# Optimization experiments

Hardware: AMD Instinct MI355X
Metric: run time of the kernel (lower is better)

The kernel has to match this reference:

```python
import jax, jax.numpy as jnp
import numpy as np

N = 50000        # nodes
E = 800000       # edges
IN_FEAT = 128
OUT_FEAT = 64
HEADS = 4
NUM_CLASSES = 40
NEG_SLOPE = 0.2  # DGL GATConv default


def setup_inputs() -> dict:
    key = jax.random.key(0)
    ks = jax.random.split(key, 12)
    x = jax.random.normal(ks[0], (N, IN_FEAT), dtype=jnp.float32)
    src = jax.random.randint(ks[1], (E,), 0, N, dtype=jnp.int32)
    dst = jax.random.randint(ks[2], (E,), 0, N, dtype=jnp.int32)
    # layer 1 params: fc W1 [in, H*D], attn_l/attn_r [H, D], bias [H*D]
    s1 = 1.0 / np.sqrt(IN_FEAT)
    W1 = jax.random.normal(ks[3], (IN_FEAT, HEADS * OUT_FEAT), dtype=jnp.float32) * s1
    al1 = jax.random.normal(ks[4], (HEADS, OUT_FEAT), dtype=jnp.float32) * 0.1
    ar1 = jax.random.normal(ks[5], (HEADS, OUT_FEAT), dtype=jnp.float32) * 0.1
    b1 = jnp.zeros((HEADS * OUT_FEAT,), dtype=jnp.float32)
    # layer 2 params: fc W2 [H*D, C], attn [1, C], bias [C]
    hid = HEADS * OUT_FEAT
    s2 = 1.0 / np.sqrt(hid)
    W2 = jax.random.normal(ks[6], (hid, NUM_CLASSES), dtype=jnp.float32) * s2
    al2 = jax.random.normal(ks[7], (1, NUM_CLASSES), dtype=jnp.float32) * 0.1
    ar2 = jax.random.normal(ks[8], (1, NUM_CLASSES), dtype=jnp.float32) * 0.1
    b2 = jnp.zeros((NUM_CLASSES,), dtype=jnp.float32)
    return {"x": x, "src": src, "dst": dst,
            "W1": W1, "al1": al1, "ar1": ar1, "b1": b1,
            "W2": W2, "al2": al2, "ar2": ar2, "b2": b2}


def gat_layer(x, W, al, ar, bias, src, dst, heads, out_feat):
    n = x.shape[0]
    h = (x @ W).reshape(n, heads, out_feat)            # [N,H,D]
    el = jnp.sum(h * al[None], axis=-1)                # [N,H]
    er = jnp.sum(h * ar[None], axis=-1)                # [N,H]
    e = el[src] + er[dst]                              # [E,H]
    e = jnp.where(e > 0, e, NEG_SLOPE * e)             # LeakyReLU
    # segment softmax over edges sharing the same destination
    emax = jax.ops.segment_max(e, dst, num_segments=n)           # [N,H]
    emax = jnp.where(jnp.isfinite(emax), emax, 0.0)              # isolated nodes
    ee = jnp.exp(e - emax[dst])                                  # [E,H]
    denom = jax.ops.segment_sum(ee, dst, num_segments=n)         # [N,H]
    denom = jnp.where(denom > 0, denom, 1.0)
    alpha = ee / denom[dst]                                      # [E,H]
    msg = h[src] * alpha[:, :, None]                             # [E,H,D]
    out = jax.ops.segment_sum(msg, dst, num_segments=n)          # [N,H,D]
    return out + bias.reshape(1, heads, out_feat)


def reference(x, src, dst, W1, al1, ar1, b1, W2, al2, ar2, b2):
    h = gat_layer(x, W1, al1, ar1, b1, src, dst, HEADS, OUT_FEAT)  # [N,H,D]
    h = h.reshape(h.shape[0], HEADS * OUT_FEAT)
    h = jax.nn.elu(h)
    h = gat_layer(h, W2, al2, ar2, b2, src, dst, 1, NUM_CLASSES)   # [N,1,C]
    return jnp.squeeze(h, axis=1)                                   # [N,C]
```

## Files before the change

kernel.cpp:

```cpp
#include <hip/hip_runtime.h>

#define NN 50000
#define NE 800000
#define HID 256
#define NCLS 40

typedef short bf16x8 __attribute__((ext_vector_type(8)));
typedef float f32x4 __attribute__((ext_vector_type(4)));

__device__ inline unsigned short f2bf(float f) {
    unsigned int u = __float_as_uint(f);
    return (unsigned short)((u + 0x7FFFu + ((u >> 16) & 1u)) >> 16);
}
__device__ inline unsigned int pack2bf(float a, float b) {
    return (unsigned int)f2bf(a) | ((unsigned int)f2bf(b) << 16);
}
__device__ inline float2 bf2x(unsigned int u) {
    return make_float2(__uint_as_float(u << 16), __uint_as_float(u & 0xFFFF0000u));
}

__global__ void k_scanA(const int* __restrict__ counts, int* __restrict__ indptr,
                        int* __restrict__ bsum) {
    __shared__ int sh[256];
    int t = threadIdx.x;
    int idx = blockIdx.x * 256 + t;
    int c = idx < NN ? counts[idx] : 0;
    sh[t] = c;
    __syncthreads();
    for (int off = 1; off < 256; off <<= 1) {
        int v = (t >= off) ? sh[t - off] : 0;
        __syncthreads();
        sh[t] += v;
        __syncthreads();
    }
    if (idx < NN) indptr[idx] = sh[t] - c;
    if (t == 255) bsum[blockIdx.x] = sh[255];
}

__global__ void k_scanB(int* __restrict__ bsum, int nb) {
    __shared__ int sh[256];
    int t = threadIdx.x;
    int c = t < nb ? bsum[t] : 0;
    sh[t] = c;
    __syncthreads();
    for (int off = 1; off < 256; off <<= 1) {
        int v = (t >= off) ? sh[t - off] : 0;
        __syncthreads();
        sh[t] += v;
        __syncthreads();
    }
    if (t < nb) bsum[t] = sh[t] - c;
}

__global__ void k_scanC(int* __restrict__ indptr, const int* __restrict__ bsum,
                        int* __restrict__ fill) {
    int idx = blockIdx.x * 256 + threadIdx.x;
    if (idx < NN) {
        indptr[idx] += bsum[idx >> 8];
        fill[idx] = 0;
    }
    if (idx == 0) indptr[NN] = NE;
}

__global__ void k_scatterw(const int* __restrict__ src, const int* __restrict__ dst,
                           const int* __restrict__ indptr, int* __restrict__ fill,
                           const float* __restrict__ el1, const float* __restrict__ er1,
                           int* __restrict__ srcs, float4* __restrict__ w4) {
    int e = blockIdx.x * 256 + threadIdx.x;
    if (e < NE) {
        int d = dst[e];
        int s = src[e];
        int pos = atomicAdd(&fill[d], 1);
        int j = indptr[d] + pos;
        srcs[j] = s;
        float4 ls = *(const float4*)&el1[(size_t)s * 4];
        float4 rd = *(const float4*)&er1[(size_t)d * 4];
        float e0 = ls.x + rd.x, e1 = ls.y + rd.y, e2 = ls.z + rd.z, e3 = ls.w + rd.w;
        e0 = e0 > 0.f ? e0 : 0.2f * e0;
        e1 = e1 > 0.f ? e1 : 0.2f * e1;
        e2 = e2 > 0.f ? e2 : 0.2f * e2;
        e3 = e3 > 0.f ? e3 : 0.2f * e3;
        w4[j] = make_float4(__expf(e0), __expf(e1), __expf(e2), __expf(e3));
    }
}

__global__ void k_prep(const float* __restrict__ W1, const float* __restrict__ al,
                       const float* __restrict__ ar, const float* __restrict__ W2,
                       float* __restrict__ wel, float* __restrict__ wer,
                       unsigned short* __restrict__ W1Tb,
                       unsigned short* __restrict__ W2Tb,
                       int* __restrict__ counts) {
    int gid = blockIdx.x * 256 + threadIdx.x;
    int nth = gridDim.x * 256;
    const int TOT = 512 + 32768 + 48 * 256;
    for (int i = gid; i < TOT; i += nth) {
        if (i < 512) {
            int k = i >> 2, h = i & 3;
            float a = 0.f, b = 0.f;
            for (int dd = 0; dd < 64; ++dd) {
                float w = W1[k * 256 + h * 64 + dd];
                a = fmaf(w, al[h * 64 + dd], a);
                b = fmaf(w, ar[h * 64 + dd], b);
            }
            wel[i] = a;
            wer[i] = b;
        } else if (i < 512 + 32768) {
            int j = i - 512;
            int col = j >> 7, k = j & 127;
            W1Tb[j] = f2bf(W1[k * 256 + col]);
        } else {
            int j = i - 512 - 32768;
            int col = j >> 8, kk = j & 255;
            W2Tb[j] = (col < NCLS) ? f2bf(W2[kk * 40 + col]) : (unsigned short)0;
        }
    }
    for (int i = gid; i < NN; i += nth) counts[i] = 0;
}

__global__ void k_elr1x(const float* __restrict__ x, const float* __restrict__ wel,
                        const float* __restrict__ wer, float* __restrict__ el1,
                        float* __restrict__ er1, unsigned short* __restrict__ xb,
                        const int* __restrict__ dst, int* __restrict__ counts) {
    __shared__ float xs[64 * 129];
    __shared__ float wels[512], wers[512];
    int t = threadIdx.x;
    int n0 = blockIdx.x * 64;
    wels[t] = wel[t]; wels[256 + t] = wel[256 + t];
    wers[t] = wer[t]; wers[256 + t] = wer[256 + t];
    for (int i = 0; i < 8; ++i) {
        int f = i * 256 + t;
        int row = f >> 5;
        int col4 = (f & 31) * 4;
        float4 v = make_float4(0.f, 0.f, 0.f, 0.f);
        if (n0 + row < NN) v = ((const float4*)x)[(size_t)n0 * 32 + f];
        xs[row * 129 + col4 + 0] = v.x;
        xs[row * 129 + col4 + 1] = v.y;
        xs[row * 129 + col4 + 2] = v.z;
        xs[row * 129 + col4 + 3] = v.w;
    }
    __syncthreads();
    int node = t & 63;
    int h = t >> 6;
    float a = 0.f, b = 0.f;
    for (int k = 0; k < 128; ++k) {
        float xv = xs[node * 129 + k];
        a = fmaf(xv, wels[k * 4 + h], a);
        b = fmaf(xv, wers[k * 4 + h], b);
    }
    if (n0 + node < NN) {
        el1[(size_t)(n0 + node) * 4 + h] = a;
        er1[(size_t)(n0 + node) * 4 + h] = b;
    }
    for (int i = 0; i < 4; ++i) {
        int g = (i * 256 + t) * 8;
        int row = g >> 7, col = g & 127;
        if (n0 + row < NN) {
            ushort4 lo, hi;
            lo.x = f2bf(xs[row * 129 + col + 0]);
            lo.y = f2bf(xs[row * 129 + col + 1]);
            lo.z = f2bf(xs[row * 129 + col + 2]);
            lo.w = f2bf(xs[row * 129 + col + 3]);
            hi.x = f2bf(xs[row * 129 + col + 4]);
            hi.y = f2bf(xs[row * 129 + col + 5]);
            hi.z = f2bf(xs[row * 129 + col + 6]);
            hi.w = f2bf(xs[row * 129 + col + 7]);
            *(ushort4*)&xb[(size_t)(n0 + row) * 128 + col] = lo;
            *(ushort4*)&xb[(size_t)(n0 + row) * 128 + col + 4] = hi;
        }
    }
    int gid = blockIdx.x * 256 + t;
    int nth = gridDim.x * 256;
    for (int e = gid; e < NE; e += nth) atomicAdd(&counts[dst[e]], 1);
}

#define XG_STRIDE 260
#define EB_STRIDE 264
#define FMA8(AC0, AC1, AC2, AC3, WQ, XV) \
    AC0.x = fmaf(WQ.x, XV.x, AC0.x); AC0.y = fmaf(WQ.x, XV.y, AC0.y); \
    AC1.x = fmaf(WQ.y, XV.x, AC1.x); AC1.y = fmaf(WQ.y, XV.y, AC1.y); \
    AC2.x = fmaf(WQ.z, XV.x, AC2.x); AC2.y = fmaf(WQ.z, XV.y, AC2.y); \
    AC3.x = fmaf(WQ.w, XV.x, AC3.x); AC3.y = fmaf(WQ.w, XV.y, AC3.y);

__global__ void k_agg1m(const unsigned int* __restrict__ xb32,
                        const float4* __restrict__ w4,
                        const int* __restrict__ indptr, const int* __restrict__ srcs,
                        const unsigned short* __restrict__ W1Tb,
                        const unsigned short* __restrict__ W2Tb,
                        const float* __restrict__ b1,
                        const float* __restrict__ al2, const float* __restrict__ ar2,
                        unsigned short* __restrict__ h2b,
                        float* __restrict__ el2, float* __restrict__ er2) {
    __shared__ unsigned int xg[16 * XG_STRIDE];
    __shared__ __align__(16) unsigned char pool[10496];
    float4 (*sw)[64] = (float4(*)[64])pool;
    int (*si)[64] = (int(*)[64])(pool + 8192);
    unsigned short* eb = (unsigned short*)pool;
    float* pel = (float*)(pool + 8448);
    float* per_ = (float*)(pool + 8640);
    int t = threadIdx.x;
    int wv = t >> 6, l = t & 63;
    int n0 = blockIdx.x * 16;
    int d0 = n0 + wv * 4;
    int ip[5];
#pragma unroll
    for (int q = 0; q < 5; ++q) ip[q] = indptr[d0 + q];
    int w2 = wv * 2;
#pragma unroll
    for (int p = 0; p < 2; ++p) {
        int begA = ip[2 * p + 0], endA = ip[2 * p + 1];
        int begB = ip[2 * p + 1], endB = ip[2 * p + 2];
        int degA = endA - begA, degB = endB - begB;
        int sA = 0, sB = 0;
        float4 wA = make_float4(0.f, 0.f, 0.f, 0.f);
        float4 wB = make_float4(0.f, 0.f, 0.f, 0.f);
        if (l < degA) { sA = srcs[begA + l]; wA = w4[begA + l]; }
        if (l < degB) { sB = srcs[begB + l]; wB = w4[begB + l]; }
        si[w2 + 0][l] = sA; sw[w2 + 0][l] = wA;
        si[w2 + 1][l] = sB; sw[w2 + 1][l] = wB;
        float2 aA0 = {0,0}, aA1 = {0,0}, aA2 = {0,0}, aA3 = {0,0};
        float2 aB0 = {0,0}, aB1 = {0,0}, aB2 = {0,0}, aB3 = {0,0};
        int capA = degA < 64 ? degA : 64;
        int capB = degB < 64 ? degB : 64;
        int mcap = capA > capB ? capA : capB;
        for (int e = 0; e < mcap; e += 8) {
            unsigned int uA[8], uB[8];
            bool doA = e < capA, doB = e < capB;
            if (doA) {
#pragma unroll
                for (int q = 0; q < 8; ++q)
                    uA[q] = xb32[(size_t)si[w2][e + q] * 64 + l];
            }
            if (doB) {
#pragma unroll
                for (int q = 0; q < 8; ++q)
                    uB[q] = xb32[(size_t)si[w2 + 1][e + q] * 64 + l];
            }
            if (doA) {
#pragma unroll
                for (int q = 0; q < 8; ++q) {
                    float4 wq = sw[w2][e + q];
                    float2 xv = bf2x(uA[q]);
                    FMA8(aA0, aA1, aA2, aA3, wq, xv)
                }
            }
            if (doB) {
#pragma unroll
                for (int q = 0; q < 8; ++q) {
                    float4 wq = sw[w2 + 1][e + q];
                    float2 xv = bf2x(uB[q]);
                    FMA8(aB0, aB1, aB2, aB3, wq, xv)
                }
            }
        }
        for (int j = begA + 64; j < endA; ++j) {
            float4 wq = w4[j];
            float2 xv = bf2x(xb32[(size_t)srcs[j] * 64 + l]);
            FMA8(aA0, aA1, aA2, aA3, wq, xv)
        }
        for (int j = begB + 64; j < endB; ++j) {
            float4 wq = w4[j];
            float2 xv = bf2x(xb32[(size_t)srcs[j] * 64 + l]);
            FMA8(aB0, aB1, aB2, aB3, wq, xv)
        }
        float dA0 = wA.x, dA1 = wA.y, dA2 = wA.z, dA3 = wA.w;
        float dB0 = wB.x, dB1 = wB.y, dB2 = wB.z, dB3 = wB.w;
        for (int j = begA + 64 + l; j < endA; j += 64) {
            float4 wt = w4[j];
            dA0 += wt.x; dA1 += wt.y; dA2 += wt.z; dA3 += wt.w;
        }
        for (int j = begB + 64 + l; j < endB; j += 64) {
            float4 wt = w4[j];
            dB0 += wt.x; dB1 += wt.y; dB2 += wt.z; dB3 += wt.w;
        }
#pragma unroll
        for (int off = 32; off > 0; off >>= 1) {
            dA0 += __shfl_xor(dA0, off); dA1 += __shfl_xor(dA1, off);
            dA2 += __shfl_xor(dA2, off); dA3 += __shfl_xor(dA3, off);
            dB0 += __shfl_xor(dB0, off); dB1 += __shfl_xor(dB1, off);
            dB2 += __shfl_xor(dB2, off); dB3 += __shfl_xor(dB3, off);
        }
        float iA0 = dA0 > 0.f ? 1.f / dA0 : 0.f;
        float iA1 = dA1 > 0.f ? 1.f / dA1 : 0.f;
        float iA2 = dA2 > 0.f ? 1.f / dA2 : 0.f;
        float iA3 = dA3 > 0.f ? 1.f / dA3 : 0.f;
        float iB0 = dB0 > 0.f ? 1.f / dB0 : 0.f;
        float iB1 = dB1 > 0.f ? 1.f / dB1 : 0.f;
        float iB2 = dB2 > 0.f ? 1.f / dB2 : 0.f;
        float iB3 = dB3 > 0.f ? 1.f / dB3 : 0.f;
        unsigned int* xgA = &xg[(wv * 4 + 2 * p + 0) * XG_STRIDE];
        xgA[0 * 64 + l] = pack2bf(aA0.x * iA0, aA0.y * iA0);
        xgA[1 * 64 + l] = pack2bf(aA1.x * iA1, aA1.y * iA1);
        xgA[2 * 64 + l] = pack2bf(aA2.x * iA2, aA2.y * iA2);
        xgA[3 * 64 + l] = pack2bf(aA3.x * iA3, aA3.y * iA3);
        unsigned int* xgB = &xg[(wv * 4 + 2 * p + 1) * XG_STRIDE];
        xgB[0 * 64 + l] = pack2bf(aB0.x * iB0, aB0.y * iB0);
        xgB[1 * 64 + l] = pack2bf(aB1.x * iB1, aB1.y * iB1);
        xgB[2 * 64 + l] = pack2bf(aB2.x * iB2, aB2.y * iB2);
        xgB[3 * 64 + l] = pack2bf(aB3.x * iB3, aB3.y * iB3);
    }
    __syncthreads();
    int lrow = l & 15, lk = l >> 4;
    {
        f32x4 acc[4] = {};
#pragma unroll
        for (int kt = 0; kt < 4; ++kt) {
            bf16x8 av = *(const bf16x8*)&xg[lrow * XG_STRIDE + wv * 64 + kt * 16 + lk * 4];
#pragma unroll
            for (int nt = 0; nt < 4; ++nt) {
                int col = wv * 64 + nt * 16 + lrow;
                bf16x8 bv = *(const bf16x8*)&W1Tb[(size_t)col * 128 + kt * 32 + lk * 8];
                acc[nt] = __builtin_amdgcn_mfma_f32_16x16x32_bf16(av, bv, acc[nt], 0, 0, 0);
            }
        }
#pragma unroll
        for (int nt = 0; nt < 4; ++nt) {
            int col = wv * 64 + nt * 16 + lrow;
            float bv1 = b1[col];
#pragma unroll
            for (int r = 0; r < 4; ++r) {
                int rloc = lk * 4 + r;
                float o = acc[nt][r] + bv1;
                o = o > 0.f ? o : (__expf(o) - 1.f);
                eb[rloc * EB_STRIDE + col] = f2bf(o);
            }
        }
    }
    __syncthreads();
    if (wv < 3) {
        f32x4 acc2 = {};
#pragma unroll
        for (int kt = 0; kt < 8; ++kt) {
            bf16x8 av = *(const bf16x8*)&eb[lrow * EB_STRIDE + kt * 32 + lk * 8];
            bf16x8 bv = *(const bf16x8*)&W2Tb[(size_t)(wv * 16 + lrow) * 256 + kt * 32 + lk * 8];
            acc2 = __builtin_amdgcn_mfma_f32_16x16x32_bf16(av, bv, acc2, 0, 0, 0);
        }
        int col2 = wv * 16 + lrow;
        float alc = col2 < NCLS ? al2[col2] : 0.f;
        float arc = col2 < NCLS ? ar2[col2] : 0.f;
#pragma unroll
        for (int r = 0; r < 4; ++r) {
            int row = n0 + lk * 4 + r;
            float v = acc2[r];
            if (col2 < NCLS) h2b[(size_t)row * NCLS + col2] = f2bf(v);
            float pa = v * alc, pb = v * arc;
#pragma unroll
            for (int off = 1; off < 16; off <<= 1) {
                pa += __shfl_xor(pa, off);
                pb += __shfl_xor(pb, off);
            }
            if (lrow == 0) {
                pel[wv * 16 + lk * 4 + r] = pa;
                per_[wv * 16 + lk * 4 + r] = pb;
            }
        }
    }
    __syncthreads();
    if (t < 16) {
        el2[n0 + t] = pel[t] + pel[16 + t] + pel[32 + t];
        er2[n0 + t] = per_[t] + per_[16 + t] + per_[32 + t];
    }
}

__global__ void k_agg2(const unsigned int* __restrict__ h2b32,
                       const float* __restrict__ el2,
                       const float* __restrict__ er2, const float* __restrict__ b2,
                       const int* __restrict__ indptr, const int* __restrict__ srcs,
                       float* __restrict__ out) {
    __shared__ int   si[8][64];
    __shared__ float sw[8][64];
    int t = threadIdx.x;
    int wv = t >> 6, l = t & 63;
    int dA = blockIdx.x * 8 + wv * 2;
    int dB = dA + 1;
    int begA = indptr[dA], endA = indptr[dA + 1];
    int begB = endA, endB = indptr[dB + 1];
    int degA = endA - begA, degB = endB - begB;
    float rdA = er2[dA], rdB = er2[dB];
    int sA = 0, sB = 0;
    float wA = 0.f, wB = 0.f;
    if (l < degA) {
        sA = srcs[begA + l];
        float e = el2[sA] + rdA;
        e = e > 0.f ? e : 0.2f * e;
        wA = __expf(e);
    }
    if (l < degB) {
        sB = srcs[begB + l];
        float e = el2[sB] + rdB;
        e = e > 0.f ? e : 0.2f * e;
        wB = __expf(e);
    }
    int w2 = wv * 2;
    si[w2 + 0][l] = sA; sw[w2 + 0][l] = wA;
    si[w2 + 1][l] = sB; sw[w2 + 1][l] = wB;
    float denA = wA, denB = wB;
    for (int j = begA + 64 + l; j < endA; j += 64) {
        float e = el2[srcs[j]] + rdA;
        e = e > 0.f ? e : 0.2f * e;
        denA += __expf(e);
    }
    for (int j = begB + 64 + l; j < endB; j += 64) {
        float e = el2[srcs[j]] + rdB;
        e = e > 0.f ? e : 0.2f * e;
        denB += __expf(e);
    }
    int half = l >> 5, il = l & 31;
    bool act = il < 20;
    float2 accA = {0.f, 0.f}, accB = {0.f, 0.f};
    int capA = degA < 64 ? degA : 64;
    int capB = degB < 64 ? degB : 64;
    int mcap = capA > capB ? capA : capB;
    for (int e = 0; e < mcap; e += 8) {
        bool doA = e < capA, doB = e < capB;
        int ixA[4], ixB[4];
        float wsA[4], wsB[4];
        unsigned int uA[4], uB[4];
        if (doA) {
#pragma unroll
            for (int q = 0; q < 4; ++q) {
                int idx = e + 2 * q + half;
                ixA[q] = si[w2][idx];
                wsA[q] = sw[w2][idx];
            }
        }
        if (doB) {
#pragma unroll
            for (int q = 0; q < 4; ++q) {
                int idx = e + 2 * q + half;
                ixB[q] = si[w2 + 1][idx];
                wsB[q] = sw[w2 + 1][idx];
            }
        }
        if (doA) {
#pragma unroll
            for (int q = 0; q < 4; ++q)
                uA[q] = act ? h2b32[(size_t)ixA[q] * 20 + il] : 0u;
        }
        if (doB) {
#pragma unroll
            for (int q = 0; q < 4; ++q)
                uB[q] = act ? h2b32[(size_t)ixB[q] * 20 + il] : 0u;
        }
        if (doA) {
#pragma unroll
            for (int q = 0; q < 4; ++q) {
                float2 xv = bf2x(uA[q]);
                accA.x = fmaf(wsA[q], xv.x, accA.x);
                accA.y = fmaf(wsA[q], xv.y, accA.y);
            }
        }
        if (doB) {
#pragma unroll
            for (int q = 0; q < 4; ++q) {
                float2 xv = bf2x(uB[q]);
                accB.x = fmaf(wsB[q], xv.x, accB.x);
                accB.y = fmaf(wsB[q], xv.y, accB.y);
            }
        }
    }
    for (int j = begA + 64; j < endA; ++j) {
        int s = srcs[j];
        float e = el2[s] + rdA;
        e = e > 0.f ? e : 0.2f * e;
        float ww = (half == 0) ? __expf(e) : 0.f;
        unsigned int u = act ? h2b32[(size_t)s * 20 + il] : 0u;
        float2 xv = bf2x(u);
        accA.x = fmaf(ww, xv.x, accA.x);
        accA.y = fmaf(ww, xv.y, accA.y);
    }
    for (int j = begB + 64; j < endB; ++j) {
        int s = srcs[j];
        float e = el2[s] + rdB;
        e = e > 0.f ? e : 0.2f * e;
        float ww = (half == 0) ? __expf(e) : 0.f;
        unsigned int u = act ? h2b32[(size_t)s * 20 + il] : 0u;
        float2 xv = bf2x(u);
        accB.x = fmaf(ww, xv.x, accB.x);
        accB.y = fmaf(ww, xv.y, accB.y);
    }
#pragma unroll
    for (int off = 32; off > 0; off >>= 1) {
        denA += __shfl_xor(denA, off);
        denB += __shfl_xor(denB, off);
    }
    float invA = denA > 0.f ? 1.f / denA : 0.f;
    float invB = denB > 0.f ? 1.f / denB : 0.f;
    accA.x += __shfl_xor(accA.x, 32);
    accA.y += __shfl_xor(accA.y, 32);
    accB.x += __shfl_xor(accB.x, 32);
    accB.y += __shfl_xor(accB.y, 32);
    if (half == 0 && act) {
        float2 bb = *(const float2*)&b2[2 * il];
        *(float2*)&out[(size_t)dA * NCLS + 2 * il] =
            make_float2(fmaf(accA.x, invA, bb.x), fmaf(accA.y, invA, bb.y));
        *(float2*)&out[(size_t)dB * NCLS + 2 * il] =
            make_float2(fmaf(accB.x, invB, bb.x), fmaf(accB.y, invB, bb.y));
    }
}

extern "C" void kernel_launch(void* const* d_in, const int* in_sizes, int n_in,
                              void* d_out, int out_size, void* d_ws, size_t ws_size,
                              hipStream_t stream) {
    const float* x   = (const float*)d_in[0];
    const int*   src = (const int*)d_in[1];
    const int*   dst = (const int*)d_in[2];
    const float* W1  = (const float*)d_in[3];
    const float* al1 = (const float*)d_in[4];
    const float* ar1 = (const float*)d_in[5];
    const float* b1  = (const float*)d_in[6];
    const float* W2  = (const float*)d_in[7];
    const float* al2 = (const float*)d_in[8];
    const float* ar2 = (const float*)d_in[9];
    const float* b2  = (const float*)d_in[10];
    float* out = (float*)d_out;

    float* ws = (float*)d_ws;
    size_t off = 0;
    unsigned short* xb    = (unsigned short*)(ws + off); off += (size_t)NN * 64;
    unsigned short* h2b   = (unsigned short*)(ws + off); off += (size_t)NN * 20;
    float* el1  = ws + off; off += (size_t)NN * 4;
    float* er1  = ws + off; off += (size_t)NN * 4;
    float* el2  = ws + off; off += NN;
    float* er2  = ws + off; off += NN;
    float* wel  = ws + off; off += 512;
    float* wer  = ws + off; off += 512;
    unsigned short* w1tb = (unsigned short*)(ws + off); off += 16384;
    unsigned short* w2tb = (unsigned short*)(ws + off); off += 48 * 128;
    float* w4   = ws + off; off += (size_t)NE * 4;
    int* counts = (int*)(ws + off);
    int* indptr = counts + NN;
    int* fill   = indptr + NN + 1;
    int* srcs   = fill + NN;
    int* bsum   = srcs + NE;

    const int NB = (NN + 255) / 256;

    k_prep<<<48, 256, 0, stream>>>(W1, al1, ar1, W2, wel, wer, w1tb, w2tb, counts);
    k_elr1x<<<(NN + 63) / 64, 256, 0, stream>>>(x, wel, wer, el1, er1, xb, dst, counts);
    k_scanA<<<NB, 256, 0, stream>>>(counts, indptr, bsum);
    k_scanB<<<1, 256, 0, stream>>>(bsum, NB);
    k_scanC<<<NB, 256, 0, stream>>>(indptr, bsum, fill);
    k_scatterw<<<(NE + 255) / 256, 256, 0, stream>>>(src, dst, indptr, fill,
                                                     el1, er1, srcs, (float4*)w4);
    k_agg1m<<<NN / 16, 256, 0, stream>>>((const unsigned int*)xb, (const float4*)w4,
                                         indptr, srcs, w1tb, w2tb, b1, al2, ar2,
                                         h2b, el2, er2);

    k_agg2<<<NN / 8, 256, 0, stream>>>((const unsigned int*)h2b, el2, er2, b2,
                                       indptr, srcs, out);
}
```

Before: 197.6 us.

## Sort destination nodes by in-degree to balance aggregation workloads

Builds a degree histogram during the scan, prefix-sums it, and counting-sorts the node ids into a permutation grouped by in-degree. Both aggregation kernels then assign each wave or block a group of nodes with similar degree, which cuts the divergence and idle lanes that come from mixing short and long neighbour lists. In exchange it adds global atomics for the histogram and placement, and indirection reads. Node outputs are now scattered writes rather than contiguous ones, and locality across neighbouring nodes' indptr entries is lost.

```diff
diff --git a/kernel.cpp b/kernel.cpp
--- a/kernel.cpp
+++ b/kernel.cpp
@@ -20,7 +20,7 @@
 }
 
 __global__ void k_scanA(const int* __restrict__ counts, int* __restrict__ indptr,
-                        int* __restrict__ bsum) {
+                        int* __restrict__ bsum, int* __restrict__ dhist) {
     __shared__ int sh[256];
     int t = threadIdx.x;
     int idx = blockIdx.x * 256 + t;
@@ -33,11 +33,15 @@
         sh[t] += v;
         __syncthreads();
     }
-    if (idx < NN) indptr[idx] = sh[t] - c;
+    if (idx < NN) {
+        indptr[idx] = sh[t] - c;
+        int b = c < 255 ? c : 255;
+        atomicAdd(&dhist[b], 1);
+    }
     if (t == 255) bsum[blockIdx.x] = sh[255];
 }
 
-__global__ void k_scanB(int* __restrict__ bsum, int nb) {
+__global__ void k_scanB(int* __restrict__ bsum, int nb, int* __restrict__ dhist) {
     __shared__ int sh[256];
     int t = threadIdx.x;
     int c = t < nb ? bsum[t] : 0;
@@ -50,14 +54,31 @@
         __syncthreads();
     }
     if (t < nb) bsum[t] = sh[t] - c;
+    __syncthreads();
+    int h = dhist[t];
+    sh[t] = h;
+    __syncthreads();
+    for (int off = 1; off < 256; off <<= 1) {
+        int v = (t >= off) ? sh[t - off] : 0;
+        __syncthreads();
+        sh[t] += v;
+        __syncthreads();
+    }
+    dhist[t] = sh[t] - h;
 }
 
 __global__ void k_scanC(int* __restrict__ indptr, const int* __restrict__ bsum,
-                        int* __restrict__ fill) {
+                        int* __restrict__ fill, const int* __restrict__ counts,
+                        const int* __restrict__ dhist, int* __restrict__ dfill,
+                        int* __restrict__ perm) {
     int idx = blockIdx.x * 256 + threadIdx.x;
     if (idx < NN) {
         indptr[idx] += bsum[idx >> 8];
         fill[idx] = 0;
+        int c = counts[idx];
+        int b = c < 255 ? c : 255;
+        int pos = atomicAdd(&dfill[b], 1);
+        perm[dhist[b] + pos] = idx;
     }
     if (idx == 0) indptr[NN] = NE;
 }
@@ -89,7 +110,8 @@
                        float* __restrict__ wel, float* __restrict__ wer,
                        unsigned short* __restrict__ W1Tb,
                        unsigned short* __restrict__ W2Tb,
-                       int* __restrict__ counts) {
+                       int* __restrict__ counts, int* __restrict__ dhist,
+                       int* __restrict__ dfill) {
     int gid = blockIdx.x * 256 + threadIdx.x;
     int nth = gridDim.x * 256;
     const int TOT = 512 + 32768 + 48 * 256;
@@ -115,6 +137,7 @@
         }
     }
     for (int i = gid; i < NN; i += nth) counts[i] = 0;
+    if (gid < 256) { dhist[gid] = 0; dfill[gid] = 0; }
 }
 
 __global__ void k_elr1x(const float* __restrict__ x, const float* __restrict__ wel,
@@ -184,6 +207,7 @@
 __global__ void k_agg1m(const unsigned int* __restrict__ xb32,
                         const float4* __restrict__ w4,
                         const int* __restrict__ indptr, const int* __restrict__ srcs,
+                        const int* __restrict__ perm,
                         const unsigned short* __restrict__ W1Tb,
                         const unsigned short* __restrict__ W2Tb,
                         const float* __restrict__ b1,
@@ -192,6 +216,7 @@
                         float* __restrict__ el2, float* __restrict__ er2) {
     __shared__ unsigned int xg[16 * XG_STRIDE];
     __shared__ __align__(16) unsigned char pool[10496];
+    __shared__ int pp[16];
     float4 (*sw)[64] = (float4(*)[64])pool;
     int (*si)[64] = (int(*)[64])(pool + 8192);
     unsigned short* eb = (unsigned short*)pool;
@@ -201,14 +226,20 @@
     int wv = t >> 6, l = t & 63;
     int n0 = blockIdx.x * 16;
     int d0 = n0 + wv * 4;
-    int ip[5];
-#pragma unroll
-    for (int q = 0; q < 5; ++q) ip[q] = indptr[d0 + q];
+    if (t < 16) pp[t] = perm[n0 + t];
+    int pm4[4], ipb[4], ipe[4];
+#pragma unroll
+    for (int q = 0; q < 4; ++q) pm4[q] = perm[d0 + q];
+#pragma unroll
+    for (int q = 0; q < 4; ++q) {
+        ipb[q] = indptr[pm4[q]];
+        ipe[q] = indptr[pm4[q] + 1];
+    }
     int w2 = wv * 2;
 #pragma unroll
     for (int p = 0; p < 2; ++p) {
-        int begA = ip[2 * p + 0], endA = ip[2 * p + 1];
-        int begB = ip[2 * p + 1], endB = ip[2 * p + 2];
+        int begA = ipb[2 * p + 0], endA = ipe[2 * p + 0];
+        int begB = ipb[2 * p + 1], endB = ipe[2 * p + 1];
         int degA = endA - begA, degB = endB - begB;
         int sA = 0, sB = 0;
         float4 wA = make_float4(0.f, 0.f, 0.f, 0.f);
@@ -339,7 +370,8 @@
         float arc = col2 < NCLS ? ar2[col2] : 0.f;
 #pragma unroll
         for (int r = 0; r < 4; ++r) {
-            int row = n0 + lk * 4 + r;
+            int rloc = lk * 4 + r;
+            int row = pp[rloc];
             float v = acc2[r];
             if (col2 < NCLS) h2b[(size_t)row * NCLS + col2] = f2bf(v);
             float pa = v * alc, pb = v * arc;
@@ -349,15 +381,16 @@
                 pb += __shfl_xor(pb, off);
             }
             if (lrow == 0) {
-                pel[wv * 16 + lk * 4 + r] = pa;
-                per_[wv * 16 + lk * 4 + r] = pb;
+                pel[wv * 16 + rloc] = pa;
+                per_[wv * 16 + rloc] = pb;
             }
         }
     }
     __syncthreads();
     if (t < 16) {
-        el2[n0 + t] = pel[t] + pel[16 + t] + pel[32 + t];
-        er2[n0 + t] = per_[t] + per_[16 + t] + per_[32 + t];
+        int row = pp[t];
+        el2[row] = pel[t] + pel[16 + t] + pel[32 + t];
+        er2[row] = per_[t] + per_[16 + t] + per_[32 + t];
     }
 }
 
@@ -365,15 +398,17 @@
                        const float* __restrict__ el2,
                        const float* __restrict__ er2, const float* __restrict__ b2,
                        const int* __restrict__ indptr, const int* __restrict__ srcs,
+                       const int* __restrict__ perm,
                        float* __restrict__ out) {
     __shared__ int   si[8][64];
     __shared__ float sw[8][64];
     int t = threadIdx.x;
     int wv = t >> 6, l = t & 63;
-    int dA = blockIdx.x * 8 + wv * 2;
-    int dB = dA + 1;
+    int base8 = blockIdx.x * 8;
+    int dA = perm[base8 + wv * 2];
+    int dB = perm[base8 + wv * 2 + 1];
     int begA = indptr[dA], endA = indptr[dA + 1];
-    int begB = endA, endB = indptr[dB + 1];
+    int begB = indptr[dB], endB = indptr[dB + 1];
     int degA = endA - begA, degB = endB - begB;
     float rdA = er2[dA], rdB = er2[dB];
     int sA = 0, sB = 0;
@@ -532,20 +567,24 @@
     int* fill   = indptr + NN + 1;
     int* srcs   = fill + NN;
     int* bsum   = srcs + NE;
+    int* dhist  = bsum + 256;
+    int* dfill  = dhist + 256;
+    int* perm   = dfill + 256;
 
     const int NB = (NN + 255) / 256;
 
-    k_prep<<<48, 256, 0, stream>>>(W1, al1, ar1, W2, wel, wer, w1tb, w2tb, counts);
+    k_prep<<<48, 256, 0, stream>>>(W1, al1, ar1, W2, wel, wer, w1tb, w2tb,
+                                   counts, dhist, dfill);
     k_elr1x<<<(NN + 63) / 64, 256, 0, stream>>>(x, wel, wer, el1, er1, xb, dst, counts);
-    k_scanA<<<NB, 256, 0, stream>>>(counts, indptr, bsum);
-    k_scanB<<<1, 256, 0, stream>>>(bsum, NB);
-    k_scanC<<<NB, 256, 0, stream>>>(indptr, bsum, fill);
+    k_scanA<<<NB, 256, 0, stream>>>(counts, indptr, bsum, dhist);
+    k_scanB<<<1, 256, 0, stream>>>(bsum, NB, dhist);
+    k_scanC<<<NB, 256, 0, stream>>>(indptr, bsum, fill, counts, dhist, dfill, perm);
     k_scatterw<<<(NE + 255) / 256, 256, 0, stream>>>(src, dst, indptr, fill,
                                                      el1, er1, srcs, (float4*)w4);
     k_agg1m<<<NN / 16, 256, 0, stream>>>((const unsigned int*)xb, (const float4*)w4,
-                                         indptr, srcs, w1tb, w2tb, b1, al2, ar2,
+                                         indptr, srcs, perm, w1tb, w2tb, b1, al2, ar2,
                                          h2b, el2, er2);
 
     k_agg2<<<NN / 8, 256, 0, stream>>>((const unsigned int*)h2b, el2, er2, b2,
-                                       indptr, srcs, out);
-}
+                                       indptr, srcs, perm, out);
+}
```

New measurement: 447.2 us. +126.3%, slower.
